# Performance work log

Hardware: AMD Instinct MI355X
Metric: run time of the kernel (lower is better)

Reference implementation:

```python
import jax, jax.numpy as jnp
import numpy as np

H, QP, VP, D, DP = 4, 4, 4, 128, 64
DH = D // H


def setup_inputs() -> dict:
    key = jax.random.key(0)
    ks = jax.random.split(key, 16)
    B, L = 1, 1024
    w_c0 = float(np.log(np.e - 1.0))
    inp = {
        'single': jax.random.normal(ks[0], (B, L, D), jnp.float32),
        'pair': jax.random.normal(ks[1], (B, L, L, DP), jnp.float32),
        'T': jax.random.normal(ks[2], (B, L, 4, 4), jnp.float32),
        'w_C': jnp.full((H,), w_c0, jnp.float32),
        'ln_g': jnp.ones((D,), jnp.float32),
        'ln_b': jnp.zeros((D,), jnp.float32),
        'Wq': jax.random.normal(ks[3], (D, H * DH), jnp.float32) * 0.05,
        'Wk': jax.random.normal(ks[4], (D, H * DH), jnp.float32) * 0.05,
        'Wv': jax.random.normal(ks[5], (D, H * DH), jnp.float32) * 0.05,
        'Wqpt': jax.random.normal(ks[6], (D, H * QP * 3), jnp.float32) * 0.05,
        'Wkpt': jax.random.normal(ks[7], (D, H * QP * 3), jnp.float32) * 0.05,
        'Wvpt': jax.random.normal(ks[8], (D, H * VP * 3), jnp.float32) * 0.05,
        'Wb': jax.random.normal(ks[9], (DP, H), jnp.float32) * 0.05,
        'Wout': jax.random.normal(ks[10], (H * (DH + DP + VP * 3 + VP), D), jnp.float32) * 0.05,
        'b_out': jnp.zeros((D,), jnp.float32),
    }
    return inp


def _layernorm(x, g, b, eps=1e-5):
    x32 = x.astype(jnp.float32)
    mu = x32.mean(-1, keepdims=True)
    var = ((x32 - mu) ** 2).mean(-1, keepdims=True)
    return ((x32 - mu) * jax.lax.rsqrt(var + eps) * g + b).astype(x.dtype)


def reference(single, pair, T, w_C, ln_g, ln_b, Wq, Wk, Wv, Wqpt, Wkpt, Wvpt, Wb, Wout, b_out):
    B, L, Dm = single.shape
    scale_attn = DH ** (-0.5)
    z = _layernorm(single, ln_g, ln_b)
    Q = (z @ Wq).reshape(B, L, H, DH)
    K = (z @ Wk).reshape(B, L, H, DH)
    V = (z @ Wv).reshape(B, L, H, DH)
    Q_pt = (z @ Wqpt).reshape(B, L, H, QP, 3)
    K_pt = (z @ Wkpt).reshape(B, L, H, QP, 3)
    V_pt = (z @ Wvpt).reshape(B, L, H, VP, 3)
    R = T[..., :3, :3]   # [B,L,3,3]
    t = T[..., :3, 3]    # [B,L,3]
    # global-frame points: R @ p + t
    Q_g = jnp.einsum('blxy,blhpy->blhpx', R, Q_pt) + t[:, :, None, None, :]
    K_g = jnp.einsum('blxy,blhpy->blhpx', R, K_pt) + t[:, :, None, None, :]
    V_g = jnp.einsum('blxy,blhpy->blhpx', R, V_pt) + t[:, :, None, None, :]
    # scalar QK score [B,H,L,L]
    s_attn = jnp.einsum('bihd,bjhd->bhij', Q, K) * scale_attn
    # pair bias [B,H,L,L]
    b_attn = jnp.einsum('bijc,ch->bhij', pair, Wb)
    # squared point distance [B,H,L,L]
    diff = Q_g[:, :, None] - K_g[:, None]          # [B,L,L,H,QP,3]
    d2 = jnp.moveaxis((diff ** 2).sum((-1, -2)), -1, 1)
    w_pt = jax.nn.softplus(w_C)[None, :, None, None]
    attn = jax.nn.softmax(s_attn + b_attn - 0.5 * w_pt * d2, axis=-1)
    # scalar values [B,L,H*DH]
    o_s = jnp.einsum('bhij,bjhd->bihd', attn, V).reshape(B, L, H * DH)
    # point values aggregated in global frame then mapped back: R^T (p - t)
    o_pt_g = jnp.einsum('bhij,bjhpx->bihpx', attn, V_g)
    o_pt = jnp.einsum('blyx,blhpy->blhpx', R, o_pt_g - t[:, :, None, None, :])
    o_pt_n = jnp.sqrt((o_pt ** 2).sum(-1))
    # pair aggregation [B,L,H*DP]
    o_pair = jnp.einsum('bhij,bijc->bihc', attn, pair).reshape(B, L, H * DP)
    out = jnp.concatenate([o_s, o_pair, o_pt.reshape(B, L, -1), o_pt_n.reshape(B, L, -1)], axis=-1)
    return single + out @ Wout + b_out
```

## Files before the change

### kernel.cpp

```cpp
#include <hip/hip_runtime.h>
#include <math.h>

#define L_SEQ 1024
#define DM 128
#define JC 32
#define NCH (L_SEQ / JC)

#define OFF_KHAT 0
#define OFF_QHAT (L_SEQ * 192)
#define OFF_V    (OFF_QHAT + L_SEQ * 192)
#define OFF_VG   (OFF_V + L_SEQ * DM)

typedef __attribute__((address_space(1))) const void* gas_t;
typedef __attribute__((address_space(3))) void* las_t;

__device__ __forceinline__ void async16(const float4* g, float4* l) {
    __builtin_amdgcn_global_load_lds((gas_t)g, (las_t)l, 16, 0, 0);
}
#define ASYNC_BAR() asm volatile("s_waitcnt lgkmcnt(0)\n\ts_barrier" ::: "memory")

__global__ __launch_bounds__(256) void ipa_prep(
    const float* __restrict__ single, const float* __restrict__ T,
    const float* __restrict__ w_C, const float* __restrict__ ln_g, const float* __restrict__ ln_b,
    const float* __restrict__ Wq, const float* __restrict__ Wk, const float* __restrict__ Wv,
    const float* __restrict__ Wqpt, const float* __restrict__ Wkpt, const float* __restrict__ Wvpt,
    float* __restrict__ ws)
{
    __shared__ float z_lds[4][128];
    __shared__ float proj[4][528];
    __shared__ float qg[4][4][4][3];
    __shared__ float kg[4][4][4][3];
    __shared__ float cq[4][4], ck[4][4];

    const int t = threadIdx.x;
    const int wv = t >> 6, lane = t & 63;
    const int i0 = blockIdx.x << 2;
    const int i = i0 + wv;

    float x0 = single[i*DM + lane];
    float x1 = single[i*DM + 64 + lane];
    float s = x0 + x1, s2 = x0*x0 + x1*x1;
    #pragma unroll
    for (int off = 1; off < 64; off <<= 1) { s += __shfl_xor(s, off); s2 += __shfl_xor(s2, off); }
    float mu = s * 0.0078125f;
    float var = s2 * 0.0078125f - mu*mu;
    float rs = rsqrtf(var + 1e-5f);
    z_lds[wv][lane]      = (x0 - mu) * rs * ln_g[lane]      + ln_b[lane];
    z_lds[wv][lane + 64] = (x1 - mu) * rs * ln_g[lane + 64] + ln_b[lane + 64];
    __syncthreads();

    for (int cc = t; cc < 528; cc += 256) {
        const float* W; int col, ncol;
        if (cc < 128)      { W = Wq;   col = cc;       ncol = 128; }
        else if (cc < 256) { W = Wk;   col = cc - 128; ncol = 128; }
        else if (cc < 384) { W = Wv;   col = cc - 256; ncol = 128; }
        else if (cc < 432) { W = Wqpt; col = cc - 384; ncol = 48;  }
        else if (cc < 480) { W = Wkpt; col = cc - 432; ncol = 48;  }
        else               { W = Wvpt; col = cc - 480; ncol = 48;  }
        float a0 = 0.f, a1 = 0.f, a2 = 0.f, a3 = 0.f;
        #pragma unroll 8
        for (int k = 0; k < 128; ++k) {
            float w = W[k*ncol + col];
            a0 = fmaf(z_lds[0][k], w, a0);
            a1 = fmaf(z_lds[1][k], w, a1);
            a2 = fmaf(z_lds[2][k], w, a2);
            a3 = fmaf(z_lds[3][k], w, a3);
        }
        proj[0][cc] = a0; proj[1][cc] = a1; proj[2][cc] = a2; proj[3][cc] = a3;
    }
    __syncthreads();

    if (t < 64) {
        int r = t >> 4, h = (t >> 2) & 3, p = t & 3;
        int ii = i0 + r;
        float R[3][3], tt[3];
        #pragma unroll
        for (int x = 0; x < 3; ++x) {
            #pragma unroll
            for (int y = 0; y < 3; ++y) R[x][y] = T[ii*16 + x*4 + y];
            tt[x] = T[ii*16 + x*4 + 3];
        }
        int base = 384 + (h*4 + p)*3;
        float q0 = proj[r][base],    q1 = proj[r][base+1],  q2 = proj[r][base+2];
        float k0 = proj[r][base+48], k1 = proj[r][base+49], k2 = proj[r][base+50];
        float v0 = proj[r][base+96], v1 = proj[r][base+97], v2 = proj[r][base+98];
        #pragma unroll
        for (int x = 0; x < 3; ++x) {
            float qq = R[x][0]*q0 + R[x][1]*q1 + R[x][2]*q2 + tt[x];
            float kk = R[x][0]*k0 + R[x][1]*k1 + R[x][2]*k2 + tt[x];
            float vv = R[x][0]*v0 + R[x][1]*v1 + R[x][2]*v2 + tt[x];
            qg[r][h][p][x] = qq;
            kg[r][h][p][x] = kk;
            ws[OFF_VG + ii*48 + h*12 + p*3 + x] = vv;
        }
    }
    __syncthreads();

    if (t < 32) {
        int r = t >> 3, h = (t >> 1) & 3, isk = t & 1;
        float w = w_C[h];
        float wp = log1pf(__expf(w));
        float sq = 0.f;
        #pragma unroll
        for (int p = 0; p < 4; ++p)
            #pragma unroll
            for (int x = 0; x < 3; ++x) {
                float g = isk ? kg[r][h][p][x] : qg[r][h][p][x];
                sq += g*g;
            }
        float c = -0.5f * wp * sq;
        if (isk) ck[r][h] = c; else cq[r][h] = c;
    }
    __syncthreads();

    for (int idx = t; idx < 512; idx += 256) {
        int r = idx >> 7, d = idx & 127;
        ws[OFF_V + (size_t)(i0 + r)*DM + d] = proj[r][256 + d];
    }
    const float scale_attn = 0.17677669529663687f;
    for (int idx = t; idx < 768; idx += 256) {
        int r = idx / 192, rem = idx % 192;
        int h = rem / 48, k = rem % 48;
        int ii = i0 + r;
        float w = w_C[h];
        float wp = log1pf(__expf(w));
        float kv, qv;
        if (k < 32) {
            kv = proj[r][128 + h*32 + k];
            qv = scale_attn * proj[r][h*32 + k];
        } else if (k < 44) {
            int e = k - 32;
            kv = kg[r][h][e/3][e%3];
            qv = wp * qg[r][h][e/3][e%3];
        } else if (k == 44) { kv = ck[r][h]; qv = 1.0f; }
        else if (k == 45)   { kv = 1.0f;    qv = cq[r][h]; }
        else                { kv = 0.f;     qv = 0.f; }
        ws[OFF_KHAT + (size_t)ii*192 + h*48 + k] = kv;
        ws[OFF_QHAT + (size_t)ii*192 + h*48 + k] = qv;
    }
}

__global__ __launch_bounds__(256, 2) void ipa_attn(
    const float* __restrict__ single, const float* __restrict__ pair,
    const float* __restrict__ T, const float* __restrict__ Wb,
    const float* __restrict__ Wout, const float* __restrict__ b_out,
    const float* __restrict__ ws, float* __restrict__ out)
{
    __shared__ __align__(16) float4 pair_lds[2][JC][16];
    __shared__ __align__(16) float4 p4_lds[JC];
    __shared__ float alpha_lds[4];
    __shared__ float l_lds[4];
    __shared__ __align__(16) float4 qhat_lds[4][12];
    __shared__ __align__(16) float4 wbt_lds[4][16];

    const int t = threadIdx.x;
    const int wv = t >> 6, lane = t & 63;
    const int i = blockIdx.x;

    if (t < 48) ((float4*)qhat_lds)[t] = ((const float4*)(ws + OFF_QHAT))[(size_t)i*48 + t];
    else if (t < 112) {
        int c = t - 48;
        float4 w = ((const float4*)Wb)[c];
        float* wf = (float*)wbt_lds;
        wf[0*64 + c] = w.x; wf[1*64 + c] = w.y; wf[2*64 + c] = w.z; wf[3*64 + c] = w.w;
    }

    const int j_s  = lane & 31, khalf = lane >> 5;
    const int d4   = lane & 7,  jg_s  = lane >> 3;
    const int c4p  = lane >> 4, jg_p  = lane & 15;
    const int g4   = lane & 3,  jg_g  = lane >> 2;
    const int g4c  = (g4 < 3) ? g4 : 0;
    const int c4o  = wv << 2;

    float m_run = -INFINITY, l_run = 0.f;
    float alpha_own = 0.f;
    float4 accp[4];
    float4 accs;
    float4 accg;
    accs = make_float4(0.f,0.f,0.f,0.f);
    accg = make_float4(0.f,0.f,0.f,0.f);
    #pragma unroll
    for (int h = 0; h < 4; ++h) accp[h] = make_float4(0.f,0.f,0.f,0.f);

    const float4* pair4 = (const float4*)pair;
    const float4* kh4   = (const float4*)(ws + OFF_KHAT);
    const float4* v4    = (const float4*)(ws + OFF_V);
    const float4* vg4   = (const float4*)(ws + OFF_VG);
    float4* plds_flat   = &pair_lds[0][0][0];
    float*  p_s         = (float*)p4_lds;

    #pragma unroll
    for (int it = 0; it < 2; ++it) {
        int idx = it*256 + t;
        int j = idx >> 4, slot = idx & 15;
        int c4 = slot ^ (j & 7);
        async16(pair4 + ((size_t)i*L_SEQ + j)*16 + c4, plds_flat + idx);
    }

    for (int ch = 0; ch < NCH; ++ch) {
        const int cur = ch & 1;
        const int j0 = ch * JC;

        ASYNC_BAR();
        if (ch + 1 < NCH) {
            const int jn = (ch + 1) * JC;
            #pragma unroll
            for (int it = 0; it < 2; ++it) {
                int idx = it*256 + t;
                int j = idx >> 4, slot = idx & 15;
                int c4 = slot ^ (j & 7);
                async16(pair4 + ((size_t)i*L_SEQ + jn + j)*16 + c4,
                        plds_flat + (1 - cur)*512 + idx);
            }
            asm volatile("s_waitcnt vmcnt(2)" ::: "memory");
        } else {
            asm volatile("s_waitcnt vmcnt(0)" ::: "memory");
        }
        ASYNC_BAR();

        float4 kh[6];
        {
            const float4* kp = kh4 + (size_t)(j0 + j_s)*48 + wv*12 + khalf*6;
            #pragma unroll
            for (int k4 = 0; k4 < 6; ++k4) kh[k4] = kp[k4];
        }

        float4 vv[4];
        float4 gvv[2];

        {
            float bias = 0.f;
            #pragma unroll
            for (int cp = 0; cp < 8; ++cp) {
                int c4 = khalf*8 + cp;
                int sw = c4 ^ (j_s & 7);
                float4 pv = pair_lds[cur][j_s][sw];
                float4 wh = wbt_lds[wv][c4];
                bias += pv.x*wh.x + pv.y*wh.y + pv.z*wh.z + pv.w*wh.w;
            }
            float da = 0.f, db = 0.f;
            #pragma unroll
            for (int k4 = 0; k4 < 6; k4 += 2) {
                float4 q0 = qhat_lds[wv][khalf*6 + k4];
                float4 q1 = qhat_lds[wv][khalf*6 + k4 + 1];
                da = fmaf(kh[k4].x,   q0.x, da); da = fmaf(kh[k4].y,   q0.y, da);
                da = fmaf(kh[k4].z,   q0.z, da); da = fmaf(kh[k4].w,   q0.w, da);
                db = fmaf(kh[k4+1].x, q1.x, db); db = fmaf(kh[k4+1].y, q1.y, db);
                db = fmaf(kh[k4+1].z, q1.z, db); db = fmaf(kh[k4+1].w, q1.w, db);
            }
            float part = da + db + bias;
            float logit = part + __shfl_xor(part, 32);

            #pragma unroll
            for (int jj = 0; jj < 4; ++jj)
                vv[jj] = v4[(size_t)(j0 + jg_s + 8*jj)*32 + wv*8 + d4];
            #pragma unroll
            for (int jj = 0; jj < 2; ++jj)
                gvv[jj] = vg4[(size_t)(j0 + jg_g + 16*jj)*12 + wv*3 + g4c];

            float cmax = logit;
            #pragma unroll
            for (int off = 1; off < 32; off <<= 1) cmax = fmaxf(cmax, __shfl_xor(cmax, off));
            float mn = fmaxf(m_run, cmax);
            float alpha = __expf(m_run - mn);
            float p = __expf(logit - mn);
            l_run = l_run * alpha + p;
            m_run = mn;
            alpha_own = alpha;
            if (lane < 32) p_s[j_s*4 + wv] = p;
            if (lane == 0) alpha_lds[wv] = alpha;
        }
        ASYNC_BAR();

        {
            float al0 = alpha_lds[0], al1 = alpha_lds[1], al2 = alpha_lds[2], al3 = alpha_lds[3];
            accp[0].x *= al0; accp[0].y *= al0; accp[0].z *= al0; accp[0].w *= al0;
            accp[1].x *= al1; accp[1].y *= al1; accp[1].z *= al1; accp[1].w *= al1;
            accp[2].x *= al2; accp[2].y *= al2; accp[2].z *= al2; accp[2].w *= al2;
            accp[3].x *= al3; accp[3].y *= al3; accp[3].z *= al3; accp[3].w *= al3;
            accs.x *= alpha_own; accs.y *= alpha_own; accs.z *= alpha_own; accs.w *= alpha_own;
            accg.x *= alpha_own; accg.y *= alpha_own; accg.z *= alpha_own; accg.w *= alpha_own;

            {
                int c4 = c4o + c4p;
                #pragma unroll
                for (int jj = 0; jj < 2; ++jj) {
                    int j = jg_p + 16*jj;
                    int sw = c4 ^ (j & 7);
                    float4 pv = pair_lds[cur][j][sw];
                    float4 pj = p4_lds[j];
                    accp[0].x = fmaf(pj.x, pv.x, accp[0].x); accp[0].y = fmaf(pj.x, pv.y, accp[0].y);
                    accp[0].z = fmaf(pj.x, pv.z, accp[0].z); accp[0].w = fmaf(pj.x, pv.w, accp[0].w);
                    accp[1].x = fmaf(pj.y, pv.x, accp[1].x); accp[1].y = fmaf(pj.y, pv.y, accp[1].y);
                    accp[1].z = fmaf(pj.y, pv.z, accp[1].z); accp[1].w = fmaf(pj.y, pv.w, accp[1].w);
                    accp[2].x = fmaf(pj.z, pv.x, accp[2].x); accp[2].y = fmaf(pj.z, pv.y, accp[2].y);
                    accp[2].z = fmaf(pj.z, pv.z, accp[2].z); accp[2].w = fmaf(pj.z, pv.w, accp[2].w);
                    accp[3].x = fmaf(pj.w, pv.x, accp[3].x); accp[3].y = fmaf(pj.w, pv.y, accp[3].y);
                    accp[3].z = fmaf(pj.w, pv.z, accp[3].z); accp[3].w = fmaf(pj.w, pv.w, accp[3].w);
                }
            }
            #pragma unroll
            for (int jj = 0; jj < 4; ++jj) {
                int j = jg_s + 8*jj;
                float pa = p_s[j*4 + wv];
                accs.x = fmaf(pa, vv[jj].x, accs.x); accs.y = fmaf(pa, vv[jj].y, accs.y);
                accs.z = fmaf(pa, vv[jj].z, accs.z); accs.w = fmaf(pa, vv[jj].w, accs.w);
            }
            #pragma unroll
            for (int jj = 0; jj < 2; ++jj) {
                int j = jg_g + 16*jj;
                float pa = p_s[j*4 + wv];
                accg.x = fmaf(pa, gvv[jj].x, accg.x); accg.y = fmaf(pa, gvv[jj].y, accg.y);
                accg.z = fmaf(pa, gvv[jj].z, accg.z); accg.w = fmaf(pa, gvv[jj].w, accg.w);
            }
        }
    }

    #pragma unroll
    for (int h = 0; h < 4; ++h) {
        #pragma unroll
        for (int off = 1; off < 16; off <<= 1) {
            accp[h].x += __shfl_xor(accp[h].x, off);
            accp[h].y += __shfl_xor(accp[h].y, off);
            accp[h].z += __shfl_xor(accp[h].z, off);
            accp[h].w += __shfl_xor(accp[h].w, off);
        }
    }
    #pragma unroll
    for (int off = 8; off < 64; off <<= 1) {
        accs.x += __shfl_xor(accs.x, off); accs.y += __shfl_xor(accs.y, off);
        accs.z += __shfl_xor(accs.z, off); accs.w += __shfl_xor(accs.w, off);
    }
    #pragma unroll
    for (int off = 4; off < 64; off <<= 1) {
        accg.x += __shfl_xor(accg.x, off); accg.y += __shfl_xor(accg.y, off);
        accg.z += __shfl_xor(accg.z, off); accg.w += __shfl_xor(accg.w, off);
    }
    #pragma unroll
    for (int off = 1; off < 64; off <<= 1)
        l_run += __shfl_xor(l_run, off);
    if (lane == 0) l_lds[wv] = l_run * 0.5f;
    __syncthreads();

    float* scratch = (float*)&pair_lds[0][0][0];
    float* u   = scratch;
    float* og  = scratch + 448;
    float* tmp = scratch + 512;

    float invl[4];
    #pragma unroll
    for (int h = 0; h < 4; ++h) invl[h] = 1.f / l_lds[h];

    if (lane < 8) {
        float sc = invl[wv];
        int base = wv*32 + lane*4;
        u[base+0] = accs.x*sc; u[base+1] = accs.y*sc;
        u[base+2] = accs.z*sc; u[base+3] = accs.w*sc;
    }
    if ((lane & 15) == 0) {
        int c4 = c4o + (lane >> 4);
        #pragma unroll
        for (int h = 0; h < 4; ++h) {
            float sc = invl[h];
            int base = 128 + h*64 + c4*4;
            u[base+0] = accp[h].x*sc; u[base+1] = accp[h].y*sc;
            u[base+2] = accp[h].z*sc; u[base+3] = accp[h].w*sc;
        }
    }
    if (lane < 3) {
        float sc = invl[wv];
        og[wv*12 + lane*4+0] = accg.x*sc; og[wv*12 + lane*4+1] = accg.y*sc;
        og[wv*12 + lane*4+2] = accg.z*sc; og[wv*12 + lane*4+3] = accg.w*sc;
    }
    __syncthreads();

    if (t < 16) {
        int h = t >> 2, p = t & 3;
        float R[3][3], tt[3];
        #pragma unroll
        for (int x = 0; x < 3; ++x) {
            #pragma unroll
            for (int y = 0; y < 3; ++y) R[x][y] = T[i*16 + x*4 + y];
            tt[x] = T[i*16 + x*4 + 3];
        }
        float v0 = og[h*12 + p*3+0] - tt[0];
        float v1 = og[h*12 + p*3+1] - tt[1];
        float v2 = og[h*12 + p*3+2] - tt[2];
        float n2 = 0.f;
        #pragma unroll
        for (int x = 0; x < 3; ++x) {
            float o = R[0][x]*v0 + R[1][x]*v1 + R[2][x]*v2;
            u[384 + h*12 + p*3 + x] = o;
            n2 += o*o;
        }
        u[432 + h*4 + p] = sqrtf(n2);
    }
    __syncthreads();

    {
        int d = t & 127, khf = t >> 7;
        float acc = 0.f;
        const float4* u4 = (const float4*)u;
        int k0 = khf * 56;
        #pragma unroll 4
        for (int k4 = k0; k4 < k0 + 56; ++k4) {
            float4 uu = u4[k4];
            const float* wp = Wout + (size_t)(k4*4)*128 + d;
            acc = fmaf(uu.x, wp[0],   acc);
            acc = fmaf(uu.y, wp[128], acc);
            acc = fmaf(uu.z, wp[256], acc);
            acc = fmaf(uu.w, wp[384], acc);
        }
        if (khf) tmp[d] = acc;
        __syncthreads();
        if (!khf) out[i*DM + d] = single[i*DM + d] + b_out[d] + acc + tmp[d];
    }
}

extern "C" void kernel_launch(void* const* d_in, const int* in_sizes, int n_in,
                              void* d_out, int out_size, void* d_ws, size_t ws_size,
                              hipStream_t stream)
{
    const float* single = (const float*)d_in[0];
    const float* pair   = (const float*)d_in[1];
    const float* T      = (const float*)d_in[2];
    const float* w_C    = (const float*)d_in[3];
    const float* ln_g   = (const float*)d_in[4];
    const float* ln_b   = (const float*)d_in[5];
    const float* Wq     = (const float*)d_in[6];
    const float* Wk     = (const float*)d_in[7];
    const float* Wv     = (const float*)d_in[8];
    const float* Wqpt   = (const float*)d_in[9];
    const float* Wkpt   = (const float*)d_in[10];
    const float* Wvpt   = (const float*)d_in[11];
    const float* Wb     = (const float*)d_in[12];
    const float* Wout   = (const float*)d_in[13];
    const float* b_out  = (const float*)d_in[14];
    float* out = (float*)d_out;
    float* ws  = (float*)d_ws;

    ipa_prep<<<256, 256, 0, stream>>>(single, T, w_C, ln_g, ln_b, Wq, Wk, Wv, Wqpt, Wkpt, Wvpt, ws);
    ipa_attn<<<1024, 256, 0, stream>>>(single, pair, T, Wb, Wout, b_out, ws, out);
}
```

Before: 541.5 us.

## Split key range across waves with per-wave online softmax and merge

The attention kernel now gives each wave its own 256-key slice of the row, with a private double-buffered pair tile in LDS. Each wave runs an online softmax over all 4 heads, and the four partial states are merged at the end with a max/rescale combine. This removes the block-wide barriers and cross-wave alpha exchange that every 32-key chunk used to need. The prep kernel now handles one row per block with 1024 blocks instead of four rows per block. The cost is more LDS per block, global key/value loads issued without a prefetch buffer, and a final merge step.

After: 491.9 us. 1.1x faster.

```diff
diff --git a/kernel.cpp b/kernel.cpp
--- a/kernel.cpp
+++ b/kernel.cpp
@@ -3,8 +3,6 @@
 
 #define L_SEQ 1024
 #define DM 128
-#define JC 32
-#define NCH (L_SEQ / JC)
 
 #define OFF_KHAT 0
 #define OFF_QHAT (L_SEQ * 192)
@@ -17,7 +15,6 @@
 __device__ __forceinline__ void async16(const float4* g, float4* l) {
     __builtin_amdgcn_global_load_lds((gas_t)g, (las_t)l, 16, 0, 0);
 }
-#define ASYNC_BAR() asm volatile("s_waitcnt lgkmcnt(0)\n\ts_barrier" ::: "memory")
 
 __global__ __launch_bounds__(256) void ipa_prep(
     const float* __restrict__ single, const float* __restrict__ T,
@@ -26,27 +23,27 @@
     const float* __restrict__ Wqpt, const float* __restrict__ Wkpt, const float* __restrict__ Wvpt,
     float* __restrict__ ws)
 {
-    __shared__ float z_lds[4][128];
-    __shared__ float proj[4][528];
-    __shared__ float qg[4][4][4][3];
-    __shared__ float kg[4][4][4][3];
-    __shared__ float cq[4][4], ck[4][4];
+    __shared__ float z_lds[128];
+    __shared__ float proj[528];
+    __shared__ float qg[4][4][3];
+    __shared__ float kg[4][4][3];
+    __shared__ float cq[4], ck[4];
 
     const int t = threadIdx.x;
-    const int wv = t >> 6, lane = t & 63;
-    const int i0 = blockIdx.x << 2;
-    const int i = i0 + wv;
-
-    float x0 = single[i*DM + lane];
-    float x1 = single[i*DM + 64 + lane];
-    float s = x0 + x1, s2 = x0*x0 + x1*x1;
-    #pragma unroll
-    for (int off = 1; off < 64; off <<= 1) { s += __shfl_xor(s, off); s2 += __shfl_xor(s2, off); }
-    float mu = s * 0.0078125f;
-    float var = s2 * 0.0078125f - mu*mu;
-    float rs = rsqrtf(var + 1e-5f);
-    z_lds[wv][lane]      = (x0 - mu) * rs * ln_g[lane]      + ln_b[lane];
-    z_lds[wv][lane + 64] = (x1 - mu) * rs * ln_g[lane + 64] + ln_b[lane + 64];
+    const int i = blockIdx.x;
+
+    if (t < 64) {
+        float x0 = single[i*DM + t];
+        float x1 = single[i*DM + 64 + t];
+        float s = x0 + x1, s2 = x0*x0 + x1*x1;
+        #pragma unroll
+        for (int off = 1; off < 64; off <<= 1) { s += __shfl_xor(s, off); s2 += __shfl_xor(s2, off); }
+        float mu = s * 0.0078125f;
+        float var = s2 * 0.0078125f - mu*mu;
+        float rs = rsqrtf(var + 1e-5f);
+        z_lds[t]      = (x0 - mu) * rs * ln_g[t]      + ln_b[t];
+        z_lds[t + 64] = (x1 - mu) * rs * ln_g[t + 64] + ln_b[t + 64];
+    }
     __syncthreads();
 
     for (int cc = t; cc < 528; cc += 256) {
@@ -57,47 +54,41 @@
         else if (cc < 432) { W = Wqpt; col = cc - 384; ncol = 48;  }
         else if (cc < 480) { W = Wkpt; col = cc - 432; ncol = 48;  }
         else               { W = Wvpt; col = cc - 480; ncol = 48;  }
-        float a0 = 0.f, a1 = 0.f, a2 = 0.f, a3 = 0.f;
+        float a = 0.f;
         #pragma unroll 8
-        for (int k = 0; k < 128; ++k) {
-            float w = W[k*ncol + col];
-            a0 = fmaf(z_lds[0][k], w, a0);
-            a1 = fmaf(z_lds[1][k], w, a1);
-            a2 = fmaf(z_lds[2][k], w, a2);
-            a3 = fmaf(z_lds[3][k], w, a3);
-        }
-        proj[0][cc] = a0; proj[1][cc] = a1; proj[2][cc] = a2; proj[3][cc] = a3;
-    }
-    __syncthreads();
-
-    if (t < 64) {
-        int r = t >> 4, h = (t >> 2) & 3, p = t & 3;
-        int ii = i0 + r;
+        for (int k = 0; k < 128; ++k)
+            a = fmaf(z_lds[k], W[k*ncol + col], a);
+        proj[cc] = a;
+    }
+    __syncthreads();
+
+    if (t < 16) {
+        int h = t >> 2, p = t & 3;
         float R[3][3], tt[3];
         #pragma unroll
         for (int x = 0; x < 3; ++x) {
             #pragma unroll
-            for (int y = 0; y < 3; ++y) R[x][y] = T[ii*16 + x*4 + y];
-            tt[x] = T[ii*16 + x*4 + 3];
+            for (int y = 0; y < 3; ++y) R[x][y] = T[i*16 + x*4 + y];
+            tt[x] = T[i*16 + x*4 + 3];
         }
         int base = 384 + (h*4 + p)*3;
-        float q0 = proj[r][base],    q1 = proj[r][base+1],  q2 = proj[r][base+2];
-        float k0 = proj[r][base+48], k1 = proj[r][base+49], k2 = proj[r][base+50];
-        float v0 = proj[r][base+96], v1 = proj[r][base+97], v2 = proj[r][base+98];
+        float q0 = proj[base],    q1 = proj[base+1],  q2 = proj[base+2];
+        float k0 = proj[base+48], k1 = proj[base+49], k2 = proj[base+50];
+        float v0 = proj[base+96], v1 = proj[base+97], v2 = proj[base+98];
         #pragma unroll
         for (int x = 0; x < 3; ++x) {
             float qq = R[x][0]*q0 + R[x][1]*q1 + R[x][2]*q2 + tt[x];
             float kk = R[x][0]*k0 + R[x][1]*k1 + R[x][2]*k2 + tt[x];
             float vv = R[x][0]*v0 + R[x][1]*v1 + R[x][2]*v2 + tt[x];
-            qg[r][h][p][x] = qq;
-            kg[r][h][p][x] = kk;
-            ws[OFF_VG + ii*48 + h*12 + p*3 + x] = vv;
-        }
-    }
-    __syncthreads();
-
-    if (t < 32) {
-        int r = t >> 3, h = (t >> 1) & 3, isk = t & 1;
+            qg[h][p][x] = qq;
+            kg[h][p][x] = kk;
+            ws[OFF_VG + (size_t)i*48 + h*12 + p*3 + x] = vv;
+        }
+    }
+    __syncthreads();
+
+    if (t < 8) {
+        int h = t >> 1, isk = t & 1;
         float w = w_C[h];
         float wp = log1pf(__expf(w));
         float sq = 0.f;
@@ -105,38 +96,33 @@
         for (int p = 0; p < 4; ++p)
             #pragma unroll
             for (int x = 0; x < 3; ++x) {
-                float g = isk ? kg[r][h][p][x] : qg[r][h][p][x];
+                float g = isk ? kg[h][p][x] : qg[h][p][x];
                 sq += g*g;
             }
         float c = -0.5f * wp * sq;
-        if (isk) ck[r][h] = c; else cq[r][h] = c;
-    }
-    __syncthreads();
-
-    for (int idx = t; idx < 512; idx += 256) {
-        int r = idx >> 7, d = idx & 127;
-        ws[OFF_V + (size_t)(i0 + r)*DM + d] = proj[r][256 + d];
-    }
+        if (isk) ck[h] = c; else cq[h] = c;
+    }
+    __syncthreads();
+
+    if (t < 128) ws[OFF_V + (size_t)i*DM + t] = proj[256 + t];
     const float scale_attn = 0.17677669529663687f;
-    for (int idx = t; idx < 768; idx += 256) {
-        int r = idx / 192, rem = idx % 192;
-        int h = rem / 48, k = rem % 48;
-        int ii = i0 + r;
+    if (t < 192) {
+        int h = t / 48, k = t % 48;
         float w = w_C[h];
         float wp = log1pf(__expf(w));
         float kv, qv;
         if (k < 32) {
-            kv = proj[r][128 + h*32 + k];
-            qv = scale_attn * proj[r][h*32 + k];
+            kv = proj[128 + h*32 + k];
+            qv = scale_attn * proj[h*32 + k];
         } else if (k < 44) {
             int e = k - 32;
-            kv = kg[r][h][e/3][e%3];
-            qv = wp * qg[r][h][e/3][e%3];
-        } else if (k == 44) { kv = ck[r][h]; qv = 1.0f; }
-        else if (k == 45)   { kv = 1.0f;    qv = cq[r][h]; }
-        else                { kv = 0.f;     qv = 0.f; }
-        ws[OFF_KHAT + (size_t)ii*192 + h*48 + k] = kv;
-        ws[OFF_QHAT + (size_t)ii*192 + h*48 + k] = qv;
+            kv = kg[h][e/3][e%3];
+            qv = wp * qg[h][e/3][e%3];
+        } else if (k == 44) { kv = ck[h]; qv = 1.0f; }
+        else if (k == 45)   { kv = 1.0f; qv = cq[h]; }
+        else                { kv = 0.f;  qv = 0.f; }
+        ws[OFF_KHAT + (size_t)i*192 + t] = kv;
+        ws[OFF_QHAT + (size_t)i*192 + t] = qv;
     }
 }
 
@@ -146,39 +132,36 @@
     const float* __restrict__ Wout, const float* __restrict__ b_out,
     const float* __restrict__ ws, float* __restrict__ out)
 {
-    __shared__ __align__(16) float4 pair_lds[2][JC][16];
-    __shared__ __align__(16) float4 p4_lds[JC];
-    __shared__ float alpha_lds[4];
-    __shared__ float l_lds[4];
-    __shared__ __align__(16) float4 qhat_lds[4][12];
-    __shared__ __align__(16) float4 wbt_lds[4][16];
+    __shared__ __align__(16) float4 pair_w[4][2][16][16];
+    __shared__ __align__(16) float4 qhat_lds[4][13];
+    __shared__ __align__(16) float wbt_lds[4][68];
+    __shared__ __align__(16) float p_ws[4][16][4];
 
     const int t = threadIdx.x;
     const int wv = t >> 6, lane = t & 63;
     const int i = blockIdx.x;
 
-    if (t < 48) ((float4*)qhat_lds)[t] = ((const float4*)(ws + OFF_QHAT))[(size_t)i*48 + t];
-    else if (t < 112) {
+    if (t < 48) {
+        int h = t / 12, k4 = t % 12;
+        qhat_lds[h][k4] = ((const float4*)(ws + OFF_QHAT))[(size_t)i*48 + t];
+    } else if (t < 112) {
         int c = t - 48;
-        float4 w = ((const float4*)Wb)[c];
-        float* wf = (float*)wbt_lds;
-        wf[0*64 + c] = w.x; wf[1*64 + c] = w.y; wf[2*64 + c] = w.z; wf[3*64 + c] = w.w;
-    }
-
-    const int j_s  = lane & 31, khalf = lane >> 5;
-    const int d4   = lane & 7,  jg_s  = lane >> 3;
-    const int c4p  = lane >> 4, jg_p  = lane & 15;
-    const int g4   = lane & 3,  jg_g  = lane >> 2;
-    const int g4c  = (g4 < 3) ? g4 : 0;
-    const int c4o  = wv << 2;
+        float4 w4 = ((const float4*)Wb)[c];
+        wbt_lds[0][c] = w4.x; wbt_lds[1][c] = w4.y; wbt_lds[2][c] = w4.z; wbt_lds[3][c] = w4.w;
+    }
+
+    const int m_h  = lane & 3,  m_j  = lane >> 2;
+    const int os_h = lane >> 4, os_jh = (lane >> 3) & 1, os_d4 = lane & 7;
+    const int op_c4 = lane & 15, op_jq = lane >> 4;
+    const int og_he = lane & 15, og_jq = lane >> 4;
+    const bool og_act = og_he < 12;
+    const int og_h  = (og_act ? og_he : 0) / 3;
+    const int og_ix = og_act ? og_he : 0;
 
     float m_run = -INFINITY, l_run = 0.f;
-    float alpha_own = 0.f;
     float4 accp[4];
-    float4 accs;
-    float4 accg;
-    accs = make_float4(0.f,0.f,0.f,0.f);
-    accg = make_float4(0.f,0.f,0.f,0.f);
+    float4 accs = make_float4(0.f,0.f,0.f,0.f);
+    float4 accg = make_float4(0.f,0.f,0.f,0.f);
     #pragma unroll
     for (int h = 0; h < 4; ++h) accp[h] = make_float4(0.f,0.f,0.f,0.f);
 
@@ -186,191 +169,189 @@
     const float4* kh4   = (const float4*)(ws + OFF_KHAT);
     const float4* v4    = (const float4*)(ws + OFF_V);
     const float4* vg4   = (const float4*)(ws + OFF_VG);
-    float4* plds_flat   = &pair_lds[0][0][0];
-    float*  p_s         = (float*)p4_lds;
+    float4* mypair = &pair_w[wv][0][0][0];
+    const size_t prow_base = (size_t)i*L_SEQ + wv*256;
 
     #pragma unroll
-    for (int it = 0; it < 2; ++it) {
-        int idx = it*256 + t;
+    for (int it = 0; it < 4; ++it) {
+        int idx = it*64 + lane;
         int j = idx >> 4, slot = idx & 15;
         int c4 = slot ^ (j & 7);
-        async16(pair4 + ((size_t)i*L_SEQ + j)*16 + c4, plds_flat + idx);
-    }
-
-    for (int ch = 0; ch < NCH; ++ch) {
-        const int cur = ch & 1;
-        const int j0 = ch * JC;
-
-        ASYNC_BAR();
-        if (ch + 1 < NCH) {
-            const int jn = (ch + 1) * JC;
+        async16(pair4 + (prow_base + j)*16 + c4, mypair + idx);
+    }
+    __syncthreads();
+
+    for (int s = 0; s < 16; ++s) {
+        const int cur = s & 1;
+        const int j0 = wv*256 + s*16;
+
+        float4 kh[12];
+        {
+            const float4* kp = kh4 + (size_t)(j0 + m_j)*48 + m_h*12;
             #pragma unroll
-            for (int it = 0; it < 2; ++it) {
-                int idx = it*256 + t;
+            for (int k4 = 0; k4 < 12; ++k4) kh[k4] = kp[k4];
+        }
+        if (s + 1 < 16) {
+            #pragma unroll
+            for (int it = 0; it < 4; ++it) {
+                int idx = it*64 + lane;
                 int j = idx >> 4, slot = idx & 15;
                 int c4 = slot ^ (j & 7);
-                async16(pair4 + ((size_t)i*L_SEQ + jn + j)*16 + c4,
-                        plds_flat + (1 - cur)*512 + idx);
+                async16(pair4 + (prow_base + (s+1)*16 + j)*16 + c4,
+                        mypair + (1 - cur)*256 + idx);
             }
-            asm volatile("s_waitcnt vmcnt(2)" ::: "memory");
+            asm volatile("s_waitcnt vmcnt(16)" ::: "memory");
         } else {
-            asm volatile("s_waitcnt vmcnt(0)" ::: "memory");
-        }
-        ASYNC_BAR();
-
-        float4 kh[6];
-        {
-            const float4* kp = kh4 + (size_t)(j0 + j_s)*48 + wv*12 + khalf*6;
-            #pragma unroll
-            for (int k4 = 0; k4 < 6; ++k4) kh[k4] = kp[k4];
-        }
-
-        float4 vv[4];
-        float4 gvv[2];
-
-        {
-            float bias = 0.f;
-            #pragma unroll
-            for (int cp = 0; cp < 8; ++cp) {
-                int c4 = khalf*8 + cp;
-                int sw = c4 ^ (j_s & 7);
-                float4 pv = pair_lds[cur][j_s][sw];
-                float4 wh = wbt_lds[wv][c4];
-                bias += pv.x*wh.x + pv.y*wh.y + pv.z*wh.z + pv.w*wh.w;
-            }
-            float da = 0.f, db = 0.f;
-            #pragma unroll
-            for (int k4 = 0; k4 < 6; k4 += 2) {
-                float4 q0 = qhat_lds[wv][khalf*6 + k4];
-                float4 q1 = qhat_lds[wv][khalf*6 + k4 + 1];
-                da = fmaf(kh[k4].x,   q0.x, da); da = fmaf(kh[k4].y,   q0.y, da);
-                da = fmaf(kh[k4].z,   q0.z, da); da = fmaf(kh[k4].w,   q0.w, da);
-                db = fmaf(kh[k4+1].x, q1.x, db); db = fmaf(kh[k4+1].y, q1.y, db);
-                db = fmaf(kh[k4+1].z, q1.z, db); db = fmaf(kh[k4+1].w, q1.w, db);
-            }
-            float part = da + db + bias;
-            float logit = part + __shfl_xor(part, 32);
-
-            #pragma unroll
-            for (int jj = 0; jj < 4; ++jj)
-                vv[jj] = v4[(size_t)(j0 + jg_s + 8*jj)*32 + wv*8 + d4];
-            #pragma unroll
-            for (int jj = 0; jj < 2; ++jj)
-                gvv[jj] = vg4[(size_t)(j0 + jg_g + 16*jj)*12 + wv*3 + g4c];
-
-            float cmax = logit;
-            #pragma unroll
-            for (int off = 1; off < 32; off <<= 1) cmax = fmaxf(cmax, __shfl_xor(cmax, off));
-            float mn = fmaxf(m_run, cmax);
-            float alpha = __expf(m_run - mn);
-            float p = __expf(logit - mn);
-            l_run = l_run * alpha + p;
-            m_run = mn;
-            alpha_own = alpha;
-            if (lane < 32) p_s[j_s*4 + wv] = p;
-            if (lane == 0) alpha_lds[wv] = alpha;
-        }
-        ASYNC_BAR();
-
-        {
-            float al0 = alpha_lds[0], al1 = alpha_lds[1], al2 = alpha_lds[2], al3 = alpha_lds[3];
-            accp[0].x *= al0; accp[0].y *= al0; accp[0].z *= al0; accp[0].w *= al0;
-            accp[1].x *= al1; accp[1].y *= al1; accp[1].z *= al1; accp[1].w *= al1;
-            accp[2].x *= al2; accp[2].y *= al2; accp[2].z *= al2; accp[2].w *= al2;
-            accp[3].x *= al3; accp[3].y *= al3; accp[3].z *= al3; accp[3].w *= al3;
-            accs.x *= alpha_own; accs.y *= alpha_own; accs.z *= alpha_own; accs.w *= alpha_own;
-            accg.x *= alpha_own; accg.y *= alpha_own; accg.z *= alpha_own; accg.w *= alpha_own;
-
-            {
-                int c4 = c4o + c4p;
-                #pragma unroll
-                for (int jj = 0; jj < 2; ++jj) {
-                    int j = jg_p + 16*jj;
-                    int sw = c4 ^ (j & 7);
-                    float4 pv = pair_lds[cur][j][sw];
-                    float4 pj = p4_lds[j];
-                    accp[0].x = fmaf(pj.x, pv.x, accp[0].x); accp[0].y = fmaf(pj.x, pv.y, accp[0].y);
-                    accp[0].z = fmaf(pj.x, pv.z, accp[0].z); accp[0].w = fmaf(pj.x, pv.w, accp[0].w);
-                    accp[1].x = fmaf(pj.y, pv.x, accp[1].x); accp[1].y = fmaf(pj.y, pv.y, accp[1].y);
-                    accp[1].z = fmaf(pj.y, pv.z, accp[1].z); accp[1].w = fmaf(pj.y, pv.w, accp[1].w);
-                    accp[2].x = fmaf(pj.z, pv.x, accp[2].x); accp[2].y = fmaf(pj.z, pv.y, accp[2].y);
-                    accp[2].z = fmaf(pj.z, pv.z, accp[2].z); accp[2].w = fmaf(pj.z, pv.w, accp[2].w);
-                    accp[3].x = fmaf(pj.w, pv.x, accp[3].x); accp[3].y = fmaf(pj.w, pv.y, accp[3].y);
-                    accp[3].z = fmaf(pj.w, pv.z, accp[3].z); accp[3].w = fmaf(pj.w, pv.w, accp[3].w);
-                }
-            }
-            #pragma unroll
-            for (int jj = 0; jj < 4; ++jj) {
-                int j = jg_s + 8*jj;
-                float pa = p_s[j*4 + wv];
-                accs.x = fmaf(pa, vv[jj].x, accs.x); accs.y = fmaf(pa, vv[jj].y, accs.y);
-                accs.z = fmaf(pa, vv[jj].z, accs.z); accs.w = fmaf(pa, vv[jj].w, accs.w);
-            }
-            #pragma unroll
-            for (int jj = 0; jj < 2; ++jj) {
-                int j = jg_g + 16*jj;
-                float pa = p_s[j*4 + wv];
-                accg.x = fmaf(pa, gvv[jj].x, accg.x); accg.y = fmaf(pa, gvv[jj].y, accg.y);
-                accg.z = fmaf(pa, gvv[jj].z, accg.z); accg.w = fmaf(pa, gvv[jj].w, accg.w);
-            }
-        }
-    }
-
+            asm volatile("s_waitcnt vmcnt(12)" ::: "memory");
+        }
+
+        const float4* prow = mypair + cur*256 + m_j*16;
+        const float4* wrow = (const float4*)&wbt_lds[m_h][0];
+        float bias = 0.f;
+        #pragma unroll
+        for (int cc = 0; cc < 16; ++cc) {
+            int sw = cc ^ (m_j & 7);
+            float4 pv = prow[sw];
+            float4 wh = wrow[cc];
+            bias += pv.x*wh.x + pv.y*wh.y + pv.z*wh.z + pv.w*wh.w;
+        }
+        float da = 0.f, db = 0.f;
+        #pragma unroll
+        for (int k4 = 0; k4 < 12; k4 += 2) {
+            float4 qa = qhat_lds[m_h][k4], qb = qhat_lds[m_h][k4+1];
+            da = fmaf(kh[k4].x,   qa.x, da); da = fmaf(kh[k4].y,   qa.y, da);
+            da = fmaf(kh[k4].z,   qa.z, da); da = fmaf(kh[k4].w,   qa.w, da);
+            db = fmaf(kh[k4+1].x, qb.x, db); db = fmaf(kh[k4+1].y, qb.y, db);
+            db = fmaf(kh[k4+1].z, qb.z, db); db = fmaf(kh[k4+1].w, qb.w, db);
+        }
+        float logit = da + db + bias;
+
+        float cmax = logit;
+        cmax = fmaxf(cmax, __shfl_xor(cmax, 4));
+        cmax = fmaxf(cmax, __shfl_xor(cmax, 8));
+        cmax = fmaxf(cmax, __shfl_xor(cmax, 16));
+        cmax = fmaxf(cmax, __shfl_xor(cmax, 32));
+        float mn = fmaxf(m_run, cmax);
+        float alpha = __expf(m_run - mn);
+        float p = __expf(logit - mn);
+        l_run = l_run * alpha + p;
+        m_run = mn;
+        p_ws[wv][m_j][m_h] = p;
+        float a0 = __shfl(alpha, 0), a1 = __shfl(alpha, 1);
+        float a2 = __shfl(alpha, 2), a3 = __shfl(alpha, 3);
+        asm volatile("" ::: "memory");
+
+        accp[0].x *= a0; accp[0].y *= a0; accp[0].z *= a0; accp[0].w *= a0;
+        accp[1].x *= a1; accp[1].y *= a1; accp[1].z *= a1; accp[1].w *= a1;
+        accp[2].x *= a2; accp[2].y *= a2; accp[2].z *= a2; accp[2].w *= a2;
+        accp[3].x *= a3; accp[3].y *= a3; accp[3].z *= a3; accp[3].w *= a3;
+        float aa_s = (os_h & 2) ? ((os_h & 1) ? a3 : a2) : ((os_h & 1) ? a1 : a0);
+        float aa_g = (og_h & 2) ? ((og_h & 1) ? a3 : a2) : ((og_h & 1) ? a1 : a0);
+        accs.x *= aa_s; accs.y *= aa_s; accs.z *= aa_s; accs.w *= aa_s;
+        accg.x *= aa_g; accg.y *= aa_g; accg.z *= aa_g; accg.w *= aa_g;
+
+        #pragma unroll
+        for (int jj = 0; jj < 4; ++jj) {
+            int j = op_jq*4 + jj;
+            int sw = op_c4 ^ (j & 7);
+            float4 pv = mypair[cur*256 + j*16 + sw];
+            float4 pj = *(const float4*)&p_ws[wv][j][0];
+            accp[0].x = fmaf(pj.x, pv.x, accp[0].x); accp[0].y = fmaf(pj.x, pv.y, accp[0].y);
+            accp[0].z = fmaf(pj.x, pv.z, accp[0].z); accp[0].w = fmaf(pj.x, pv.w, accp[0].w);
+            accp[1].x = fmaf(pj.y, pv.x, accp[1].x); accp[1].y = fmaf(pj.y, pv.y, accp[1].y);
+            accp[1].z = fmaf(pj.y, pv.z, accp[1].z); accp[1].w = fmaf(pj.y, pv.w, accp[1].w);
+            accp[2].x = fmaf(pj.z, pv.x, accp[2].x); accp[2].y = fmaf(pj.z, pv.y, accp[2].y);
+            accp[2].z = fmaf(pj.z, pv.z, accp[2].z); accp[2].w = fmaf(pj.z, pv.w, accp[2].w);
+            accp[3].x = fmaf(pj.w, pv.x, accp[3].x); accp[3].y = fmaf(pj.w, pv.y, accp[3].y);
+            accp[3].z = fmaf(pj.w, pv.z, accp[3].z); accp[3].w = fmaf(pj.w, pv.w, accp[3].w);
+        }
+        #pragma unroll
+        for (int jj = 0; jj < 8; ++jj) {
+            int j = os_jh*8 + jj;
+            float4 vvv = v4[(size_t)(j0 + j)*32 + os_h*8 + os_d4];
+            float pa = p_ws[wv][j][os_h];
+            accs.x = fmaf(pa, vvv.x, accs.x); accs.y = fmaf(pa, vvv.y, accs.y);
+            accs.z = fmaf(pa, vvv.z, accs.z); accs.w = fmaf(pa, vvv.w, accs.w);
+        }
+        #pragma unroll
+        for (int jj = 0; jj < 4; ++jj) {
+            int j = og_jq*4 + jj;
+            float4 gv = vg4[(size_t)(j0 + j)*12 + og_ix];
+            float pa = og_act ? p_ws[wv][j][og_h] : 0.f;
+            accg.x = fmaf(pa, gv.x, accg.x); accg.y = fmaf(pa, gv.y, accg.y);
+            accg.z = fmaf(pa, gv.z, accg.z); accg.w = fmaf(pa, gv.w, accg.w);
+        }
+    }
+
+    l_run += __shfl_xor(l_run, 4);  l_run += __shfl_xor(l_run, 8);
+    l_run += __shfl_xor(l_run, 16); l_run += __shfl_xor(l_run, 32);
     #pragma unroll
     for (int h = 0; h < 4; ++h) {
         #pragma unroll
-        for (int off = 1; off < 16; off <<= 1) {
+        for (int off = 16; off < 64; off <<= 1) {
             accp[h].x += __shfl_xor(accp[h].x, off);
             accp[h].y += __shfl_xor(accp[h].y, off);
             accp[h].z += __shfl_xor(accp[h].z, off);
             accp[h].w += __shfl_xor(accp[h].w, off);
         }
     }
+    accs.x += __shfl_xor(accs.x, 8); accs.y += __shfl_xor(accs.y, 8);
+    accs.z += __shfl_xor(accs.z, 8); accs.w += __shfl_xor(accs.w, 8);
     #pragma unroll
-    for (int off = 8; off < 64; off <<= 1) {
-        accs.x += __shfl_xor(accs.x, off); accs.y += __shfl_xor(accs.y, off);
-        accs.z += __shfl_xor(accs.z, off); accs.w += __shfl_xor(accs.w, off);
-    }
-    #pragma unroll
-    for (int off = 4; off < 64; off <<= 1) {
+    for (int off = 16; off < 64; off <<= 1) {
         accg.x += __shfl_xor(accg.x, off); accg.y += __shfl_xor(accg.y, off);
         accg.z += __shfl_xor(accg.z, off); accg.w += __shfl_xor(accg.w, off);
     }
-    #pragma unroll
-    for (int off = 1; off < 64; off <<= 1)
-        l_run += __shfl_xor(l_run, off);
-    if (lane == 0) l_lds[wv] = l_run * 0.5f;
-    __syncthreads();
-
-    float* scratch = (float*)&pair_lds[0][0][0];
-    float* u   = scratch;
-    float* og  = scratch + 448;
-    float* tmp = scratch + 512;
-
-    float invl[4];
-    #pragma unroll
-    for (int h = 0; h < 4; ++h) invl[h] = 1.f / l_lds[h];
-
-    if (lane < 8) {
-        float sc = invl[wv];
-        int base = wv*32 + lane*4;
-        u[base+0] = accs.x*sc; u[base+1] = accs.y*sc;
-        u[base+2] = accs.z*sc; u[base+3] = accs.w*sc;
-    }
-    if ((lane & 15) == 0) {
-        int c4 = c4o + (lane >> 4);
-        #pragma unroll
-        for (int h = 0; h < 4; ++h) {
-            float sc = invl[h];
-            int base = 128 + h*64 + c4*4;
-            u[base+0] = accp[h].x*sc; u[base+1] = accp[h].y*sc;
-            u[base+2] = accp[h].z*sc; u[base+3] = accp[h].w*sc;
-        }
-    }
-    if (lane < 3) {
-        float sc = invl[wv];
-        og[wv*12 + lane*4+0] = accg.x*sc; og[wv*12 + lane*4+1] = accg.y*sc;
-        og[wv*12 + lane*4+2] = accg.z*sc; og[wv*12 + lane*4+3] = accg.w*sc;
+
+    float* scratch = (float*)&pair_w[0][0][0][0];
+    float* cw = scratch + wv*2048;
+    if (lane < 16) {
+        #pragma unroll
+        for (int h = 0; h < 4; ++h)
+            *(float4*)&cw[h*64 + op_c4*4] = accp[h];
+    }
+    if (os_jh == 0) *(float4*)&cw[256 + os_h*32 + os_d4*4] = accs;
+    if (lane < 12)  *(float4*)&cw[384 + lane*4] = accg;
+    if (lane < 4)   { cw[432 + lane] = l_run; cw[436 + lane] = m_run; }
+    __syncthreads();
+
+    float* u    = scratch + 1024;
+    float* og   = scratch + 1536;
+    float* tmp  = scratch + 1600;
+    float* wtS  = scratch + 1728;
+    float* invS = scratch + 1744;
+
+    if (t < 4) {
+        int h = t;
+        float m0 = scratch[436 + h],        m1 = scratch[2048 + 436 + h];
+        float m2 = scratch[4096 + 436 + h], m3 = scratch[6144 + 436 + h];
+        float M = fmaxf(fmaxf(m0, m1), fmaxf(m2, m3));
+        float w0 = __expf(m0 - M), w1 = __expf(m1 - M);
+        float w2 = __expf(m2 - M), w3 = __expf(m3 - M);
+        float L = scratch[432+h]*w0 + scratch[2048+432+h]*w1
+                + scratch[4096+432+h]*w2 + scratch[6144+432+h]*w3;
+        wtS[h] = w0; wtS[4+h] = w1; wtS[8+h] = w2; wtS[12+h] = w3;
+        invS[h] = 1.f / L;
+    }
+    __syncthreads();
+
+    {
+        int hp = t >> 6;
+        float sum = scratch[t]*wtS[hp] + scratch[2048+t]*wtS[4+hp]
+                  + scratch[4096+t]*wtS[8+hp] + scratch[6144+t]*wtS[12+hp];
+        u[128 + t] = sum * invS[hp];
+        if (t < 128) {
+            int hs = t >> 5;
+            float ssum = scratch[256+t]*wtS[hs] + scratch[2048+256+t]*wtS[4+hs]
+                       + scratch[4096+256+t]*wtS[8+hs] + scratch[6144+256+t]*wtS[12+hs];
+            u[t] = ssum * invS[hs];
+        }
+        if (t < 48) {
+            int hg = t / 12;
+            float gsum = scratch[384+t]*wtS[hg] + scratch[2048+384+t]*wtS[4+hg]
+                       + scratch[4096+384+t]*wtS[8+hg] + scratch[6144+384+t]*wtS[12+hg];
+            og[t] = gsum * invS[hg];
+        }
     }
     __syncthreads();
 
@@ -439,6 +420,6 @@
     float* out = (float*)d_out;
     float* ws  = (float*)d_ws;
 
-    ipa_prep<<<256, 256, 0, stream>>>(single, T, w_C, ln_g, ln_b, Wq, Wk, Wv, Wqpt, Wkpt, Wvpt, ws);
+    ipa_prep<<<1024, 256, 0, stream>>>(single, T, w_C, ln_g, ln_b, Wq, Wk, Wv, Wqpt, Wkpt, Wvpt, ws);
     ipa_attn<<<1024, 256, 0, stream>>>(single, pair, T, Wb, Wout, b_out, ws, out);
 }
```
